# Kernel tuning notes

Measured on AMD Instinct MI355X. Metric: run time of the kernel, lower is better.

## Reference

```python
import jax, jax.numpy as jnp
import numpy as np

K = 3          # kernel size
DIL = 1        # dilation
PAD = (K + (K - 1) * (DIL - 1)) // 2   # = 1
CENTER = (K * K - 1) // 2              # = 4
D_MIN = 0.0
D_MAX = 10.0
MIN_NGHBR = 4


def _unfold(x):
    """x: (B,C,H,W) -> patches (B,H,W,k*k,C), matching torch.nn.Unfold ordering."""
    b, c, h, w = x.shape
    xp = jnp.pad(x, ((0, 0), (0, 0), (PAD, PAD), (PAD, PAD)))
    # fixed k*k=9 taps: loop over the kernel window only (not data dims)
    pats = [xp[:, :, i * DIL:i * DIL + h, j * DIL:j * DIL + w]
            for i in range(K) for j in range(K)]
    p = jnp.stack(pats, axis=2)          # (B,C,kk,H,W)
    return p.transpose(0, 3, 4, 2, 1)    # (B,H,W,kk,C)


def setup_inputs() -> dict:
    key = jax.random.key(0)
    kxy, kz = jax.random.split(key)
    B, H, W = 4, 480, 640
    xy = jax.random.normal(kxy, (B, 2, H, W), dtype=jnp.float32)
    z = jax.random.uniform(kz, (B, 1, H, W), dtype=jnp.float32, minval=0.1, maxval=9.9)
    points = jnp.concatenate([xy, z], axis=1)  # (B,3,H,W)
    return {"points": points}


def reference(points):
    b, _, h, w = points.shape
    # 3x3 neighborhoods of 3D points: (B,H,W,9,3)
    A3 = _unfold(points)
    # depth-validity mask, unfolded over the same window: (B,H,W,9,1)
    depth = points[:, 2:3]
    valid = ((depth > D_MIN) & (depth < D_MAX)).astype(points.dtype)
    vc = _unfold(valid)
    # homogeneous design matrix A = [x y z 1], zeroed where neighbor invalid
    A = jnp.concatenate([A3, jnp.ones_like(A3[..., :1])], axis=-1)  # (B,H,W,9,4)
    A = jnp.where(vc > 0.5, A, jnp.zeros_like(A))
    # normal equations: per-pixel symmetric PSD 4x4
    AtA = jnp.einsum('bhwki,bhwkj->bhwij', A, A)
    # A^T A is symmetric PSD -> real eigensystem; eigh gives ascending eigvals,
    # so the null-space direction (smallest eigval) is column 0.
    eig_val, eig_vec = jnp.linalg.eigh(AtA)
    normal4 = eig_vec[..., :, 0]                      # (B,H,W,4)
    normal = normal4[..., :3].transpose(0, 3, 1, 2)   # (B,3,H,W)
    # F.normalize(p=2, dim=1, eps=1e-12)
    nrm = jnp.linalg.norm(normal, axis=1, keepdims=True)
    normal = normal / jnp.maximum(nrm, 1e-12)
    # orient toward the camera ray
    flip = jnp.sign(jnp.sum(normal * points, axis=1, keepdims=True))
    normal = normal * flip
    # validity masks
    vm1 = vc[:, :, :, CENTER, 0][:, None] > 0.5                 # center pixel valid
    vm2 = jnp.sum(vc[..., 0], axis=3)[:, None] >= MIN_NGHBR    # enough neighbors
    # vm3 (real eigensystem) is always True for the symmetric solve
    vm4 = jnp.linalg.norm(normal, axis=1, keepdims=True) > 0.5
    valid_mask = vm1 & vm2 & vm4
    return normal, valid_mask
```

## Files before the change

kernel.cpp:

```cpp
#include <hip/hip_runtime.h>

#define BB 4
#define HH 480
#define WW 640

__device__ __forceinline__ double det3d(double a, double b, double c,
                                        double d, double e, double f,
                                        double g, double h, double i) {
    return a * (e * i - f * h) - b * (d * i - f * g) + c * (d * h - e * g);
}

__device__ __forceinline__ double sdet3d(double a, double b, double c,
                                         double e, double f, double i) {
    return a * (e * i - f * f) + b * (2.0 * c * f - b * i) - c * c * e;
}

__device__ __forceinline__ double crcp(double d) {
    return (double)__builtin_amdgcn_rcpf((float)d);
}

__global__ __launch_bounds__(256) void d2n_kernel(const float* __restrict__ pts,
                                                  float* __restrict__ out) {
    int idx = blockIdx.x * 256 + threadIdx.x;
    if (idx >= BB * HH * WW) return;
    int x = idx % WW;
    int t1 = idx / WW;
    int y = t1 % HH;
    int b = t1 / HH;

    const size_t HW = (size_t)HH * WW;
    const float* xs = pts + ((size_t)b * 3 + 0) * HW;
    const float* ys = pts + ((size_t)b * 3 + 1) * HW;
    const float* zs = pts + ((size_t)b * 3 + 2) * HW;

    int row[3], col[3];
    bool rin[3], cin[3];
#pragma unroll
    for (int k = 0; k < 3; ++k) {
        int yy = y + k - 1, xx = x + k - 1;
        rin[k] = (unsigned)yy < HH;
        cin[k] = (unsigned)xx < WW;
        row[k] = min(max(yy, 0), HH - 1) * WW;
        col[k] = min(max(xx, 0), WW - 1);
    }
    float px[9], py[9], pz[9];
    bool inb[9];
#pragma unroll
    for (int i = 0; i < 9; ++i) {
        int r = i / 3, c = i % 3;
        int o = row[r] + col[c];
        inb[i] = rin[r] & cin[c];
        pz[i] = zs[o];
        px[i] = xs[o];
        py[i] = ys[o];
    }

    float sxx = 0.f, sxy = 0.f, sxz = 0.f, sx = 0.f;
    float syy = 0.f, syz = 0.f, sy = 0.f;
    float szz = 0.f, sz = 0.f, cnt = 0.f;
#pragma unroll
    for (int i = 0; i < 9; ++i) {
        float w = (inb[i] && pz[i] > 0.0f && pz[i] < 10.0f) ? 1.0f : 0.0f;
        float qx = px[i] * w, qy = py[i] * w, qz = pz[i] * w;
        sxx += qx * px[i]; sxy += qx * py[i]; sxz += qx * pz[i]; sx += qx;
        syy += qy * py[i]; syz += qy * pz[i]; sy += qy;
        szz += qz * pz[i]; sz += qz;
        cnt += w;
    }

    double tr = (double)sxx + (double)syy + (double)szz + (double)cnt;
    double it = crcp(tr);
    double m00 = sxx * it, m01 = sxy * it, m02 = sxz * it, m03 = sx * it;
    double m11 = syy * it, m12 = syz * it, m13 = sy * it;
    double m22 = szz * it, m23 = sz * it, m33 = cnt * it;

    double e1 = m00 + m11 + m22 + m33;
    double e2 = (m00 * m11 - m01 * m01) + (m00 * m22 - m02 * m02) +
                (m00 * m33 - m03 * m03) + (m11 * m22 - m12 * m12) +
                (m11 * m33 - m13 * m13) + (m22 * m33 - m23 * m23);
    double P0 = sdet3d(m11, m12, m13, m22, m23, m33);
    double P1 = sdet3d(m00, m02, m03, m22, m23, m33);
    double P2 = sdet3d(m00, m01, m03, m11, m13, m33);
    double P3 = sdet3d(m00, m01, m02, m11, m12, m22);
    double e3 = P0 + P1 + P2 + P3;
    double e4 = m00 * P0
              - m01 * det3d(m01, m12, m13, m02, m22, m23, m03, m23, m33)
              + m02 * det3d(m01, m11, m13, m02, m12, m23, m03, m13, m33)
              - m03 * det3d(m01, m11, m12, m02, m12, m22, m03, m13, m23);

    float e1f = (float)e1, e2f = (float)e2, e3f = (float)e3, e4f = (float)e4;
    float t31f = 3.0f * e1f, t22f = 2.0f * e2f;
    float lf = 0.0f;
#pragma unroll
    for (int itn = 0; itn < 8; ++itn) {
        float p  = (((lf - e1f) * lf + e2f) * lf - e3f) * lf + e4f;
        float dp = ((4.0f * lf - t31f) * lf + t22f) * lf - e3f;
        dp = fminf(dp, -1e-30f);
        lf = lf - p * __builtin_amdgcn_rcpf(dp);
        lf = fminf(fmaxf(lf, 0.0f), 0.26f);
    }
    double t31 = 3.0 * e1, t22 = 2.0 * e2;
    double lam = (double)lf;
#pragma unroll
    for (int itn = 0; itn < 5; ++itn) {
        double p  = (((lam - e1) * lam + e2) * lam - e3) * lam + e4;
        double dp = ((4.0 * lam - t31) * lam + t22) * lam - e3;
        dp = fmin(dp, -1e-30);
        lam = lam - p * crcp(dp);
        lam = fmin(fmax(lam, 0.0), 0.26);
    }

    double d0 = m00 - lam, d1 = m11 - lam, d2 = m22 - lam, d3 = m33 - lam;
    double C00 =  sdet3d(d1, m12, m13, d2, m23, d3);
    double C11 =  sdet3d(d0, m02, m03, d2, m23, d3);
    double C22 =  sdet3d(d0, m01, m03, d1, m13, d3);
    double C33 =  sdet3d(d0, m01, m02, d1, m12, d2);
    double C01 = -det3d(m01, m12, m13, m02, d2, m23, m03, m23, d3);
    double C02 =  det3d(m01, d1, m13, m02, m12, m23, m03, m13, d3);
    double C03 = -det3d(m01, d1, m12, m02, m12, d2, m03, m13, m23);
    double C12 = -det3d(d0, m01, m03, m02, m12, m23, m03, m13, d3);
    double C13 =  det3d(d0, m01, m02, m02, m12, d2, m03, m13, m23);
    double C23 = -det3d(d0, m01, m02, m01, d1, m12, m03, m13, m23);

    double best = fabs(C00);
    double vx = C00, vy = C01, vz = C02, vd = C00;
    double a1 = fabs(C11);
    if (a1 > best) { best = a1; vx = C01; vy = C11; vz = C12; vd = C11; }
    double a2 = fabs(C22);
    if (a2 > best) { best = a2; vx = C02; vy = C12; vz = C22; vd = C22; }
    double a3 = fabs(C33);
    if (a3 > best) { best = a3; vx = C03; vy = C13; vz = C23; vd = C33; }

    double sc = crcp(vd);
    float fx = (float)(vx * sc), fy = (float)(vy * sc), fz = (float)(vz * sc);

    float nd = fx * fx + fy * fy + fz * fz;
    float inv = __builtin_amdgcn_rsqf(fmaxf(nd, 1e-30f));
    float nx = fx * inv, ny = fy * inv, nz = fz * inv;

    int o = y * WW + x;
    float cx = px[4], cy = py[4], cz = pz[4];
    float dot = nx * cx + ny * cy + nz * cz;
    float sgn = (dot > 0.0f) ? 1.0f : ((dot < 0.0f) ? -1.0f : 0.0f);
    nx *= sgn; ny *= sgn; nz *= sgn;

    out[((size_t)b * 3 + 0) * HW + o] = nx;
    out[((size_t)b * 3 + 1) * HW + o] = ny;
    out[((size_t)b * 3 + 2) * HW + o] = nz;

    bool cvalid = (cz > 0.0f && cz < 10.0f);
    bool m = cvalid && (cnt >= 4.0f) && (nx * nx + ny * ny + nz * nz > 0.25f);
    out[(size_t)BB * 3 * HW + (size_t)b * HW + o] = m ? 1.0f : 0.0f;
}

extern "C" void kernel_launch(void* const* d_in, const int* in_sizes, int n_in,
                              void* d_out, int out_size, void* d_ws, size_t ws_size,
                              hipStream_t stream) {
    const float* pts = (const float*)d_in[0];
    float* out = (float*)d_out;
    int total = BB * HH * WW;
    d2n_kernel<<<(total + 255) / 256, 256, 0, stream>>>(pts, out);
}
```

Baseline: 84.42 us.

## Process two pixels per thread with shared loads and cheaper eigen-solve algebra

Each thread now handles two horizontally adjacent pixels. It loads a 3x4 neighbourhood (12 taps instead of 18) and writes float2 stores. The characteristic-polynomial coefficients and the adjugate cofactors are recomputed through shared 2x2 minors, the adjugate is converted to float before selection, and the double Newton iterations drop from 5 to 4. The two pixels' Newton loops are interleaved for ILP. In exchange, register pressure rises, which launch bounds of (256,2) try to contain, and there is a small accuracy risk from the fewer double iterations and the float-precision cofactors.

```diff
diff --git a/kernel.cpp b/kernel.cpp
--- a/kernel.cpp
+++ b/kernel.cpp
@@ -3,154 +3,219 @@
 #define BB 4
 #define HH 480
 #define WW 640
-
-__device__ __forceinline__ double det3d(double a, double b, double c,
-                                        double d, double e, double f,
-                                        double g, double h, double i) {
-    return a * (e * i - f * h) - b * (d * i - f * g) + c * (d * h - e * g);
-}
-
-__device__ __forceinline__ double sdet3d(double a, double b, double c,
-                                         double e, double f, double i) {
-    return a * (e * i - f * f) + b * (2.0 * c * f - b * i) - c * c * e;
-}
+#define W2 (WW / 2)
 
 __device__ __forceinline__ double crcp(double d) {
     return (double)__builtin_amdgcn_rcpf((float)d);
 }
 
-__global__ __launch_bounds__(256) void d2n_kernel(const float* __restrict__ pts,
-                                                  float* __restrict__ out) {
+__global__ __launch_bounds__(256, 2) void d2n_kernel(const float* __restrict__ pts,
+                                                     float* __restrict__ out) {
     int idx = blockIdx.x * 256 + threadIdx.x;
-    if (idx >= BB * HH * WW) return;
-    int x = idx % WW;
-    int t1 = idx / WW;
+    if (idx >= BB * HH * W2) return;
+    int xp = idx % W2;
+    int t1 = idx / W2;
     int y = t1 % HH;
     int b = t1 / HH;
+    int x0 = xp * 2;
 
     const size_t HW = (size_t)HH * WW;
     const float* xs = pts + ((size_t)b * 3 + 0) * HW;
     const float* ys = pts + ((size_t)b * 3 + 1) * HW;
     const float* zs = pts + ((size_t)b * 3 + 2) * HW;
 
-    int row[3], col[3];
-    bool rin[3], cin[3];
+    int row[3]; bool rin[3];
 #pragma unroll
     for (int k = 0; k < 3; ++k) {
-        int yy = y + k - 1, xx = x + k - 1;
+        int yy = y + k - 1;
         rin[k] = (unsigned)yy < HH;
+        row[k] = min(max(yy, 0), HH - 1) * WW;
+    }
+    int col[4]; bool cin[4];
+#pragma unroll
+    for (int k = 0; k < 4; ++k) {
+        int xx = x0 + k - 1;
         cin[k] = (unsigned)xx < WW;
-        row[k] = min(max(yy, 0), HH - 1) * WW;
         col[k] = min(max(xx, 0), WW - 1);
     }
-    float px[9], py[9], pz[9];
-    bool inb[9];
-#pragma unroll
-    for (int i = 0; i < 9; ++i) {
-        int r = i / 3, c = i % 3;
+
+    float pxv[12], pyv[12], pzv[12];
+#pragma unroll
+    for (int i = 0; i < 12; ++i) {
+        int r = i >> 2, c = i & 3;
         int o = row[r] + col[c];
-        inb[i] = rin[r] & cin[c];
-        pz[i] = zs[o];
-        px[i] = xs[o];
-        py[i] = ys[o];
-    }
-
-    float sxx = 0.f, sxy = 0.f, sxz = 0.f, sx = 0.f;
-    float syy = 0.f, syz = 0.f, sy = 0.f;
-    float szz = 0.f, sz = 0.f, cnt = 0.f;
-#pragma unroll
-    for (int i = 0; i < 9; ++i) {
-        float w = (inb[i] && pz[i] > 0.0f && pz[i] < 10.0f) ? 1.0f : 0.0f;
-        float qx = px[i] * w, qy = py[i] * w, qz = pz[i] * w;
-        sxx += qx * px[i]; sxy += qx * py[i]; sxz += qx * pz[i]; sx += qx;
-        syy += qy * py[i]; syz += qy * pz[i]; sy += qy;
-        szz += qz * pz[i]; sz += qz;
-        cnt += w;
-    }
-
-    double tr = (double)sxx + (double)syy + (double)szz + (double)cnt;
-    double it = crcp(tr);
-    double m00 = sxx * it, m01 = sxy * it, m02 = sxz * it, m03 = sx * it;
-    double m11 = syy * it, m12 = syz * it, m13 = sy * it;
-    double m22 = szz * it, m23 = sz * it, m33 = cnt * it;
-
-    double e1 = m00 + m11 + m22 + m33;
-    double e2 = (m00 * m11 - m01 * m01) + (m00 * m22 - m02 * m02) +
-                (m00 * m33 - m03 * m03) + (m11 * m22 - m12 * m12) +
-                (m11 * m33 - m13 * m13) + (m22 * m33 - m23 * m23);
-    double P0 = sdet3d(m11, m12, m13, m22, m23, m33);
-    double P1 = sdet3d(m00, m02, m03, m22, m23, m33);
-    double P2 = sdet3d(m00, m01, m03, m11, m13, m33);
-    double P3 = sdet3d(m00, m01, m02, m11, m12, m22);
-    double e3 = P0 + P1 + P2 + P3;
-    double e4 = m00 * P0
-              - m01 * det3d(m01, m12, m13, m02, m22, m23, m03, m23, m33)
-              + m02 * det3d(m01, m11, m13, m02, m12, m23, m03, m13, m33)
-              - m03 * det3d(m01, m11, m12, m02, m12, m22, m03, m13, m23);
-
-    float e1f = (float)e1, e2f = (float)e2, e3f = (float)e3, e4f = (float)e4;
-    float t31f = 3.0f * e1f, t22f = 2.0f * e2f;
-    float lf = 0.0f;
+        pzv[i] = zs[o];
+        pxv[i] = xs[o];
+        pyv[i] = ys[o];
+    }
+
+    float sxx[2], sxy[2], sxz[2], sxs[2], syy[2], syz[2], sys[2],
+          szz[2], szs[2], cnt[2];
+#pragma unroll
+    for (int u = 0; u < 2; ++u) {
+        float axx = 0.f, axy = 0.f, axz = 0.f, ax = 0.f;
+        float ayy = 0.f, ayz = 0.f, ay = 0.f;
+        float azz = 0.f, az = 0.f, ac = 0.f;
+#pragma unroll
+        for (int i = 0; i < 9; ++i) {
+            int r = i / 3, c = i % 3;
+            int j = r * 4 + c + u;
+            bool ib = rin[r] & cin[c + u];
+            float z = pzv[j];
+            float w = (ib && z > 0.0f && z < 10.0f) ? 1.0f : 0.0f;
+            float qx = pxv[j] * w, qy = pyv[j] * w, qz = z * w;
+            axx += qx * pxv[j]; axy += qx * pyv[j]; axz += qx * z; ax += qx;
+            ayy += qy * pyv[j]; ayz += qy * z; ay += qy;
+            azz += qz * z; az += qz;
+            ac += w;
+        }
+        sxx[u] = axx; sxy[u] = axy; sxz[u] = axz; sxs[u] = ax;
+        syy[u] = ayy; syz[u] = ayz; sys[u] = ay;
+        szz[u] = azz; szs[u] = az; cnt[u] = ac;
+    }
+
+    double m00[2], m01[2], m02[2], m03[2], m11[2], m12[2], m13[2],
+           m22[2], m23[2], m33[2];
+    double e1[2], e2[2], e3[2], e4[2];
+#pragma unroll
+    for (int u = 0; u < 2; ++u) {
+        double tr = (double)sxx[u] + (double)syy[u] + (double)szz[u] + (double)cnt[u];
+        double it = crcp(tr);
+        m00[u] = sxx[u] * it; m01[u] = sxy[u] * it; m02[u] = sxz[u] * it; m03[u] = sxs[u] * it;
+        m11[u] = syy[u] * it; m12[u] = syz[u] * it; m13[u] = sys[u] * it;
+        m22[u] = szz[u] * it; m23[u] = szs[u] * it; m33[u] = cnt[u] * it;
+
+        double nA = m00[u] * m11[u] - m01[u] * m01[u];
+        double nB = m22[u] * m33[u] - m23[u] * m23[u];
+        double E4 = nA * nB;
+        double P2 = m33[u] * nA, P3 = m22[u] * nA;
+        double P0 = m11[u] * nB, P1 = m00[u] * nB;
+        double E2 = nA + nB;
+
+        nA = m00[u] * m12[u] - m02[u] * m01[u];
+        nB = m12[u] * m33[u] - m23[u] * m13[u];
+        E4 -= nA * nB; P3 -= m12[u] * nA; P0 -= m12[u] * nB;
+
+        nA = m00[u] * m13[u] - m03[u] * m01[u];
+        nB = m12[u] * m23[u] - m22[u] * m13[u];
+        E4 += nA * nB; P2 -= m13[u] * nA; P0 += m13[u] * nB;
+
+        nA = m01[u] * m12[u] - m02[u] * m11[u];
+        nB = m02[u] * m33[u] - m23[u] * m03[u];
+        E4 += nA * nB; P3 += m02[u] * nA; P1 -= m02[u] * nB;
+
+        nA = m01[u] * m13[u] - m03[u] * m11[u];
+        nB = m02[u] * m23[u] - m22[u] * m03[u];
+        E4 -= nA * nB; P2 += m03[u] * nA; P1 += m03[u] * nB;
+
+        nA = m02[u] * m13[u] - m03[u] * m12[u];
+        E4 += nA * nA;
+
+        E2 += (m00[u] * m22[u] - m02[u] * m02[u]) + (m00[u] * m33[u] - m03[u] * m03[u])
+            + (m11[u] * m22[u] - m12[u] * m12[u]) + (m11[u] * m33[u] - m13[u] * m13[u]);
+        e1[u] = (m00[u] + m11[u]) + (m22[u] + m33[u]);
+        e2[u] = E2;
+        e3[u] = (P0 + P1) + (P2 + P3);
+        e4[u] = E4;
+    }
+
+    float e1f[2], e2f[2], e3f[2], e4f[2], t31f[2], t22f[2], lf[2];
+#pragma unroll
+    for (int u = 0; u < 2; ++u) {
+        e1f[u] = (float)e1[u]; e2f[u] = (float)e2[u];
+        e3f[u] = (float)e3[u]; e4f[u] = (float)e4[u];
+        t31f[u] = 3.0f * e1f[u]; t22f[u] = 2.0f * e2f[u];
+        lf[u] = 0.0f;
+    }
 #pragma unroll
     for (int itn = 0; itn < 8; ++itn) {
-        float p  = (((lf - e1f) * lf + e2f) * lf - e3f) * lf + e4f;
-        float dp = ((4.0f * lf - t31f) * lf + t22f) * lf - e3f;
-        dp = fminf(dp, -1e-30f);
-        lf = lf - p * __builtin_amdgcn_rcpf(dp);
-        lf = fminf(fmaxf(lf, 0.0f), 0.26f);
-    }
-    double t31 = 3.0 * e1, t22 = 2.0 * e2;
-    double lam = (double)lf;
-#pragma unroll
-    for (int itn = 0; itn < 5; ++itn) {
-        double p  = (((lam - e1) * lam + e2) * lam - e3) * lam + e4;
-        double dp = ((4.0 * lam - t31) * lam + t22) * lam - e3;
-        dp = fmin(dp, -1e-30);
-        lam = lam - p * crcp(dp);
-        lam = fmin(fmax(lam, 0.0), 0.26);
-    }
-
-    double d0 = m00 - lam, d1 = m11 - lam, d2 = m22 - lam, d3 = m33 - lam;
-    double C00 =  sdet3d(d1, m12, m13, d2, m23, d3);
-    double C11 =  sdet3d(d0, m02, m03, d2, m23, d3);
-    double C22 =  sdet3d(d0, m01, m03, d1, m13, d3);
-    double C33 =  sdet3d(d0, m01, m02, d1, m12, d2);
-    double C01 = -det3d(m01, m12, m13, m02, d2, m23, m03, m23, d3);
-    double C02 =  det3d(m01, d1, m13, m02, m12, m23, m03, m13, d3);
-    double C03 = -det3d(m01, d1, m12, m02, m12, d2, m03, m13, m23);
-    double C12 = -det3d(d0, m01, m03, m02, m12, m23, m03, m13, d3);
-    double C13 =  det3d(d0, m01, m02, m02, m12, d2, m03, m13, m23);
-    double C23 = -det3d(d0, m01, m02, m01, d1, m12, m03, m13, m23);
-
-    double best = fabs(C00);
-    double vx = C00, vy = C01, vz = C02, vd = C00;
-    double a1 = fabs(C11);
-    if (a1 > best) { best = a1; vx = C01; vy = C11; vz = C12; vd = C11; }
-    double a2 = fabs(C22);
-    if (a2 > best) { best = a2; vx = C02; vy = C12; vz = C22; vd = C22; }
-    double a3 = fabs(C33);
-    if (a3 > best) { best = a3; vx = C03; vy = C13; vz = C23; vd = C33; }
-
-    double sc = crcp(vd);
-    float fx = (float)(vx * sc), fy = (float)(vy * sc), fz = (float)(vz * sc);
-
-    float nd = fx * fx + fy * fy + fz * fz;
-    float inv = __builtin_amdgcn_rsqf(fmaxf(nd, 1e-30f));
-    float nx = fx * inv, ny = fy * inv, nz = fz * inv;
-
-    int o = y * WW + x;
-    float cx = px[4], cy = py[4], cz = pz[4];
-    float dot = nx * cx + ny * cy + nz * cz;
-    float sgn = (dot > 0.0f) ? 1.0f : ((dot < 0.0f) ? -1.0f : 0.0f);
-    nx *= sgn; ny *= sgn; nz *= sgn;
-
-    out[((size_t)b * 3 + 0) * HW + o] = nx;
-    out[((size_t)b * 3 + 1) * HW + o] = ny;
-    out[((size_t)b * 3 + 2) * HW + o] = nz;
-
-    bool cvalid = (cz > 0.0f && cz < 10.0f);
-    bool m = cvalid && (cnt >= 4.0f) && (nx * nx + ny * ny + nz * nz > 0.25f);
-    out[(size_t)BB * 3 * HW + (size_t)b * HW + o] = m ? 1.0f : 0.0f;
+#pragma unroll
+        for (int u = 0; u < 2; ++u) {
+            float p  = (((lf[u] - e1f[u]) * lf[u] + e2f[u]) * lf[u] - e3f[u]) * lf[u] + e4f[u];
+            float dp = ((4.0f * lf[u] - t31f[u]) * lf[u] + t22f[u]) * lf[u] - e3f[u];
+            dp = fminf(dp, -1e-30f);
+            lf[u] = lf[u] - p * __builtin_amdgcn_rcpf(dp);
+            lf[u] = fminf(fmaxf(lf[u], 0.0f), 0.26f);
+        }
+    }
+    double lam[2], t31[2], t22[2];
+#pragma unroll
+    for (int u = 0; u < 2; ++u) {
+        t31[u] = 3.0 * e1[u]; t22[u] = 2.0 * e2[u];
+        lam[u] = (double)lf[u];
+    }
+#pragma unroll
+    for (int itn = 0; itn < 4; ++itn) {
+#pragma unroll
+        for (int u = 0; u < 2; ++u) {
+            double p  = (((lam[u] - e1[u]) * lam[u] + e2[u]) * lam[u] - e3[u]) * lam[u] + e4[u];
+            double dp = ((4.0 * lam[u] - t31[u]) * lam[u] + t22[u]) * lam[u] - e3[u];
+            dp = fmin(dp, -1e-30);
+            lam[u] = lam[u] - p * crcp(dp);
+            lam[u] = fmin(fmax(lam[u], 0.0), 0.26);
+        }
+    }
+
+    float nxo[2], nyo[2], nzo[2], msk[2];
+#pragma unroll
+    for (int u = 0; u < 2; ++u) {
+        double M00 = m00[u], M01 = m01[u], M02 = m02[u], M03 = m03[u];
+        double M11 = m11[u], M12 = m12[u], M13 = m13[u];
+        double M22 = m22[u], M23 = m23[u];
+        double L = lam[u];
+        double d0 = M00 - L, d1 = M11 - L, d2 = M22 - L, d3 = m33[u] - L;
+        double s0 = d0 * d1 - M01 * M01;
+        double s1 = d0 * M12 - M01 * M02;
+        double s2 = d0 * M13 - M01 * M03;
+        double s3 = M01 * M12 - d1 * M02;
+        double s4 = M01 * M13 - d1 * M03;
+        double s5 = M02 * M13 - M12 * M03;
+        double c1 = M02 * M23 - M03 * d2;
+        double c2 = M02 * d3 - M03 * M23;
+        double c3 = M12 * M23 - M13 * d2;
+        double c4 = M12 * d3 - M13 * M23;
+        double c5 = d2 * d3 - M23 * M23;
+
+        float f00 = (float)( d1 * c5 - M12 * c4 + M13 * c3);
+        float f01 = (float)(-M01 * c5 + M02 * c4 - M03 * c3);
+        float f02 = (float)( M13 * s5 - M23 * s4 + d3 * s3);
+        float f03 = (float)(-M12 * s5 + d2 * s4 - M23 * s3);
+        float f11 = (float)( d0 * c5 - M02 * c2 + M03 * c1);
+        float f12 = (float)(-M03 * s5 + M23 * s2 - d3 * s1);
+        float f13 = (float)( M02 * s5 - d2 * s2 + M23 * s1);
+        float f22 = (float)( M03 * s4 - M13 * s2 + d3 * s0);
+        float f23 = (float)(-M02 * s4 + M12 * s2 - M23 * s0);
+        float f33 = (float)( M02 * s3 - M12 * s1 + d2 * s0);
+
+        float bb = fabsf(f00);
+        float fx = f00, fy = f01, fz = f02;
+        float a1 = fabsf(f11);
+        if (a1 > bb) { bb = a1; fx = f01; fy = f11; fz = f12; }
+        float a2 = fabsf(f22);
+        if (a2 > bb) { bb = a2; fx = f02; fy = f12; fz = f22; }
+        float a3 = fabsf(f33);
+        if (a3 > bb) { bb = a3; fx = f03; fy = f13; fz = f23; }
+
+        float nd = fx * fx + fy * fy + fz * fz;
+        float inv = __builtin_amdgcn_rsqf(fmaxf(nd, 1e-30f));
+        float nx = fx * inv, ny = fy * inv, nz = fz * inv;
+
+        float cx = pxv[5 + u], cy = pyv[5 + u], cz = pzv[5 + u];
+        float dot = nx * cx + ny * cy + nz * cz;
+        float sgn = (dot > 0.0f) ? 1.0f : ((dot < 0.0f) ? -1.0f : 0.0f);
+        nxo[u] = nx * sgn; nyo[u] = ny * sgn; nzo[u] = nz * sgn;
+
+        bool cvalid = (cz > 0.0f && cz < 10.0f);
+        bool m = cvalid && (cnt[u] >= 4.0f) &&
+                 (nxo[u] * nxo[u] + nyo[u] * nyo[u] + nzo[u] * nzo[u] > 0.25f);
+        msk[u] = m ? 1.0f : 0.0f;
+    }
+
+    int o = y * WW + x0;
+    *reinterpret_cast<float2*>(&out[((size_t)b * 3 + 0) * HW + o]) = make_float2(nxo[0], nxo[1]);
+    *reinterpret_cast<float2*>(&out[((size_t)b * 3 + 1) * HW + o]) = make_float2(nyo[0], nyo[1]);
+    *reinterpret_cast<float2*>(&out[((size_t)b * 3 + 2) * HW + o]) = make_float2(nzo[0], nzo[1]);
+    *reinterpret_cast<float2*>(&out[(size_t)BB * 3 * HW + (size_t)b * HW + o]) = make_float2(msk[0], msk[1]);
 }
 
 extern "C" void kernel_launch(void* const* d_in, const int* in_sizes, int n_in,
@@ -158,6 +223,6 @@
                               hipStream_t stream) {
     const float* pts = (const float*)d_in[0];
     float* out = (float*)d_out;
-    int total = BB * HH * WW;
+    int total = BB * HH * W2;
     d2n_kernel<<<(total + 255) / 256, 256, 0, stream>>>(pts, out);
 }
```

Measured after the change: 85.20 us. About the same (+0.9%).
